# Kernel optimization log

Hardware: AMD Instinct MI355X
Metric: run time of the kernel (lower is better)

Reference implementation:

```python
import jax, jax.numpy as jnp
import numpy as np

NC = 4        # num_components
HEADS = 24
DH = 64
D = HEADS * DH  # 1536
EPS = 1e-8


def setup_inputs() -> dict:
    key = jax.random.key(0)
    ks = jax.random.split(key, 7)
    btc, S, E = 4, 4096, 154
    w = lambda k: jax.random.normal(k, (D, D), jnp.float32) * 0.02
    return {
        "hidden_states": jax.random.normal(ks[0], (btc, S, D), jnp.float32),
        "encoder_hidden_states": jax.random.normal(ks[1], (btc, E, D), jnp.float32),
        "temperature": jnp.ones((1,), jnp.float32),
        "Wq": w(ks[2]),
        "Wk": w(ks[3]),
        "Wv": w(ks[4]),
        "Wo": w(ks[5]),
        "bo": jnp.zeros((D,), jnp.float32),
        "pad_length": 154,
    }


def reference(hidden_states, encoder_hidden_states, temperature, Wq, Wk, Wv, Wo, bo, pad_length):
    btc, S, d = hidden_states.shape          # batch*components, latent seq, hidden
    E = encoder_hidden_states.shape[1]       # encoder seq (== pad_length)
    b = btc // NC
    scale = DH ** -0.5
    residual = hidden_states

    def heads(x, L):  # [btc, L, D] -> [btc, H, L, dh]
        return x.reshape(btc, L, HEADS, DH).transpose(0, 2, 1, 3)

    q = heads(hidden_states @ Wq.T, S)
    k = heads(encoder_hidden_states @ Wk.T, E)
    v = heads(encoder_hidden_states @ Wv.T, E)

    # pad tokens are zeros projected through the same k/v weights (no bias -> zeros)
    pad_h = jnp.zeros((btc, pad_length, d), hidden_states.dtype)
    k_pad = heads(pad_h @ Wk.T, pad_length)
    v_pad = heads(pad_h @ Wv.T, pad_length)

    scores = jnp.einsum('bhsd,bhed->bhse', q, k) / (temperature[0] + EPS)
    scores_pad = jnp.einsum('bhsd,bhpd->bhsp', q, k_pad) * scale

    # cross-component softmax over dim 0
    scores = scores.reshape(NC, b, HEADS, S, E)
    scores_pad = scores_pad.reshape(NC, b, HEADS, S, pad_length)
    w = jax.nn.softmax(scores, axis=0)
    w_pad = jax.nn.softmax(scores_pad, axis=0) * (NC / pad_length) * (1.0 - w)

    weights = jnp.concatenate(
        [w.reshape(btc, HEADS, S, E), w_pad.reshape(btc, HEADS, S, pad_length)],
        axis=-1)                              # [btc, H, S, E+pad]
    v_cat = jnp.concatenate([v, v_pad], axis=2)  # [btc, H, E+pad, dh]

    out = jnp.einsum('bhse,bhed->bhsd', weights, v_cat)
    out = out.transpose(0, 2, 1, 3).reshape(btc, S, d)
    out = out @ Wo.T + bo
    return out + residual
```

## Files before the change

kernel.cpp:

```cpp
#include <hip/hip_runtime.h>

typedef __attribute__((ext_vector_type(8))) short short8;
typedef __attribute__((ext_vector_type(4))) float f32x4;
typedef __attribute__((ext_vector_type(4))) unsigned short us4;
typedef __attribute__((ext_vector_type(4))) float float4v;

#define GLB_PTR(p) ((const __attribute__((address_space(1))) void*)(p))
#define LDS_PTR(p) ((__attribute__((address_space(3))) void*)(p))

__device__ __forceinline__ unsigned short f2bf(float f) {
  unsigned int u = __float_as_uint(f);
  u += 0x7FFF + ((u >> 16) & 1);
  return (unsigned short)(u >> 16);
}

__global__ void cvt_all(const float* __restrict__ i0, const float* __restrict__ i1,
                        const float* __restrict__ i2, const float* __restrict__ i3,
                        const float* __restrict__ i4, const float* __restrict__ i5,
                        unsigned short* __restrict__ o0, unsigned short* __restrict__ o1,
                        unsigned short* __restrict__ o2, unsigned short* __restrict__ o3,
                        unsigned short* __restrict__ o4, unsigned short* __restrict__ o5) {
  const float* in; unsigned short* out; int n4;
  switch (blockIdx.y) {
    case 0:  in = i0; out = o0; n4 = 16384 * 1536 / 4; break;
    case 1:  in = i1; out = o1; n4 = 616 * 1536 / 4;   break;
    case 2:  in = i2; out = o2; n4 = 1536 * 1536 / 4;  break;
    case 3:  in = i3; out = o3; n4 = 1536 * 1536 / 4;  break;
    case 4:  in = i4; out = o4; n4 = 1536 * 1536 / 4;  break;
    default: in = i5; out = o5; n4 = 1536 * 1536 / 4;  break;
  }
  int i = blockIdx.x * blockDim.x + threadIdx.x;
  int stride = gridDim.x * blockDim.x;
  for (; i < n4; i += stride) {
    float4v v = *(const float4v*)(in + (size_t)i * 4);
    us4 o;
    o[0] = f2bf(v[0]); o[1] = f2bf(v[1]); o[2] = f2bf(v[2]); o[3] = f2bf(v[3]);
    *(us4*)(out + (size_t)i * 4) = o;
  }
}

template<int MODE>
__device__ __forceinline__ void gemm_big_body(
    const unsigned short* __restrict__ A,
    const unsigned short* __restrict__ B,
    unsigned short* __restrict__ Cb,
    float* __restrict__ Cf,
    const float* __restrict__ bias,
    const float* __restrict__ resid,
    unsigned short* smem, int bid, int tid) {
  constexpr int K = 1536, N = 1536, BK = 32, NKT = K / BK;
  unsigned short* As = smem;
  unsigned short* Bs = smem + 3 * 8192;

  const int xcd = bid & 7, idx = bid >> 3;
  const int m0 = (xcd * 8 + idx / 12) * 256;
  const int n0 = (idx % 12) * 128;

  const int w = tid >> 6, l = tid & 63, lr = l & 15, lg = l >> 4;
  const int wr = w >> 1, wc = w & 1;
  const int ga = lg ^ (lr & 3);

  const int srow = w * 16 + (l >> 2);
  const int sg = (l & 3) ^ ((l >> 2) & 3);
  const unsigned short* aSrc = A + (size_t)(m0 + srow) * K + sg * 8;
  const unsigned short* bSrc = B + (size_t)(n0 + srow) * K + sg * 8;

  f32x4 acc[4][4] = {};

  auto stage = [&](int buf, int kt) {
    const int k0 = kt * BK;
    unsigned short* AsW = As + buf * 8192 + w * 512;
    unsigned short* BsW = Bs + buf * 4096 + w * 512;
    __builtin_amdgcn_global_load_lds(GLB_PTR(aSrc + k0),                    LDS_PTR(AsW),        16, 0, 0);
    __builtin_amdgcn_global_load_lds(GLB_PTR(aSrc + (size_t)128 * K + k0),  LDS_PTR(AsW + 4096), 16, 0, 0);
    __builtin_amdgcn_global_load_lds(GLB_PTR(bSrc + k0),                    LDS_PTR(BsW),        16, 0, 0);
  };

  auto loadfrags = [&](int buf, short8* af, short8* bfv) {
    const unsigned short* Asb = As + buf * 8192;
    const unsigned short* Bsb = Bs + buf * 4096;
#pragma unroll
    for (int i = 0; i < 4; ++i)
      af[i] = *(const short8*)(Asb + (wr * 64 + i * 16 + lr) * 32 + ga * 8);
#pragma unroll
    for (int j = 0; j < 4; ++j)
      bfv[j] = *(const short8*)(Bsb + (wc * 64 + j * 16 + lr) * 32 + ga * 8);
  };

  auto mfma_all = [&](short8* af, short8* bfv) {
#pragma unroll
    for (int i = 0; i < 4; ++i)
#pragma unroll
      for (int j = 0; j < 4; ++j)
        acc[i][j] = __builtin_amdgcn_mfma_f32_16x16x32_bf16(af[i], bfv[j], acc[i][j], 0, 0, 0);
  };

  stage(0, 0); stage(1, 1); stage(2, 2);

  int cur = 0;
  for (int kt = 0; kt < NKT - 3; ++kt) {
    asm volatile("s_waitcnt vmcnt(6)" ::: "memory");
    __builtin_amdgcn_s_barrier();
    __builtin_amdgcn_sched_barrier(0);
    short8 af[4], bfv[4];
    loadfrags(cur, af, bfv);
    asm volatile("s_waitcnt lgkmcnt(0)" ::: "memory");
    __builtin_amdgcn_sched_barrier(0);
    __builtin_amdgcn_s_barrier();
    __builtin_amdgcn_sched_barrier(0);
    stage(cur, kt + 3);
    __builtin_amdgcn_s_setprio(1);
    mfma_all(af, bfv);
    __builtin_amdgcn_s_setprio(0);
    cur = cur + 1; if (cur == 3) cur = 0;
  }
#pragma unroll
  for (int j = 0; j < 3; ++j) {
    if (j == 0)      asm volatile("s_waitcnt vmcnt(6)" ::: "memory");
    else if (j == 1) asm volatile("s_waitcnt vmcnt(3)" ::: "memory");
    else             asm volatile("s_waitcnt vmcnt(0)" ::: "memory");
    __builtin_amdgcn_s_barrier();
    __builtin_amdgcn_sched_barrier(0);
    short8 af[4], bfv[4];
    loadfrags(cur, af, bfv);
    mfma_all(af, bfv);
    cur = cur + 1; if (cur == 3) cur = 0;
  }

#pragma unroll
  for (int i = 0; i < 4; ++i) {
    const int rb = m0 + wr * 64 + i * 16 + lg * 4;
#pragma unroll
    for (int j = 0; j < 4; ++j) {
      const int col = n0 + wc * 64 + j * 16 + lr;
#pragma unroll
      for (int r = 0; r < 4; ++r) {
        size_t o = (size_t)(rb + r) * N + col;
        if (MODE == 0) Cb[o] = f2bf(acc[i][j][r]);
        else           Cf[o] = acc[i][j][r] + bias[col] + resid[o];
      }
    }
  }
}

__device__ __forceinline__ void gemm_kv_body(
    const unsigned short* __restrict__ A,
    const unsigned short* __restrict__ Bk,
    const unsigned short* __restrict__ Bv,
    unsigned short* __restrict__ Ck,
    unsigned short* __restrict__ Vt,
    unsigned short* smem, int by, int tid) {
  constexpr int K = 1536, N = 1536, Mc = 615;
  unsigned short* As = smem;
  unsigned short* Bs = smem + 4096;
  const int bx = by % 5, yy = by / 5;
  const unsigned short* B = yy < 12 ? Bk : Bv;
  const int m0 = bx * 128, n0 = (yy % 12) * 128;
  const bool act = tid < 256;
  const int t = tid;
  const int w = t >> 6, l = t & 63, lr = l & 15, lg = l >> 4;
  const int wr = w >> 1, wc = w & 1;
  const int srow = t >> 2, scol = (t & 3) * 8;

  f32x4 acc[4][4] = {};
  unsigned short* AsW = As + w * 512;
  unsigned short* BsW = Bs + w * 512;
  long ar0 = m0 + srow;       if (ar0 > Mc) ar0 = Mc;
  long ar1 = m0 + srow + 64;  if (ar1 > Mc) ar1 = Mc;

  for (int k0 = 0; k0 < K; k0 += 32) {
    if (act) {
      __builtin_amdgcn_global_load_lds(GLB_PTR(A + ar0 * (long)K + k0 + scol), LDS_PTR(AsW),        16, 0, 0);
      __builtin_amdgcn_global_load_lds(GLB_PTR(A + ar1 * (long)K + k0 + scol), LDS_PTR(AsW + 2048), 16, 0, 0);
      __builtin_amdgcn_global_load_lds(GLB_PTR(B + (long)(n0 + srow) * K + k0 + scol),      LDS_PTR(BsW),        16, 0, 0);
      __builtin_amdgcn_global_load_lds(GLB_PTR(B + (long)(n0 + srow + 64) * K + k0 + scol), LDS_PTR(BsW + 2048), 16, 0, 0);
    }
    __syncthreads();
    if (act) {
      short8 af[4], bfv[4];
#pragma unroll
      for (int i = 0; i < 4; ++i) {
        af[i]  = *(const short8*)(As + (wr * 64 + i * 16 + lr) * 32 + lg * 8);
        bfv[i] = *(const short8*)(Bs + (wc * 64 + i * 16 + lr) * 32 + lg * 8);
      }
#pragma unroll
      for (int i = 0; i < 4; ++i)
#pragma unroll
        for (int j = 0; j < 4; ++j)
          acc[i][j] = __builtin_amdgcn_mfma_f32_16x16x32_bf16(af[i], bfv[j], acc[i][j], 0, 0, 0);
    }
    __syncthreads();
  }

  if (!act) return;
  if (yy < 12) {
#pragma unroll
    for (int i = 0; i < 4; ++i) {
      int rb = m0 + wr * 64 + i * 16 + lg * 4;
#pragma unroll
      for (int j = 0; j < 4; ++j) {
        int col = n0 + wc * 64 + j * 16 + lr;
#pragma unroll
        for (int r = 0; r < 4; ++r)
          Ck[(long)(rb + r) * N + col] = f2bf(acc[i][j][r]);
      }
    }
  } else {
#pragma unroll
    for (int i = 0; i < 4; ++i) {
      int rb = m0 + wr * 64 + i * 16 + lg * 4;
#pragma unroll
      for (int j = 0; j < 4; ++j) {
        int col = n0 + wc * 64 + j * 16 + lr;
        int hh = col >> 6, dd = col & 63;
#pragma unroll
        for (int r = 0; r < 4; ++r) {
          int m = rb + r;
          if (m < 616) {
            int c = (unsigned)m / 154u;
            int e = m - c * 154;
            Vt[((long)((c * 24 + hh) * 64 + dd)) * 160 + e] = f2bf(acc[i][j][r]);
          }
        }
      }
    }
  }
}

__global__ __launch_bounds__(512, 4) void gemm_q_kv(
    const unsigned short* __restrict__ HSb, const unsigned short* __restrict__ Wqb,
    unsigned short* __restrict__ Qb,
    const unsigned short* __restrict__ EHSb, const unsigned short* __restrict__ Wkb,
    const unsigned short* __restrict__ Wvb,
    unsigned short* __restrict__ Ck, unsigned short* __restrict__ Vt) {
  __shared__ unsigned short smem[36864];
  if (blockIdx.x < 768)
    gemm_big_body<0>(HSb, Wqb, Qb, nullptr, nullptr, nullptr, smem, blockIdx.x, threadIdx.x);
  else
    gemm_kv_body(EHSb, Wkb, Wvb, Ck, Vt, smem, blockIdx.x - 768, threadIdx.x);
}

__global__ __launch_bounds__(512, 4) void gemm_o(
    const unsigned short* __restrict__ Ob, const unsigned short* __restrict__ Wob,
    float* __restrict__ Cf, const float* __restrict__ bias, const float* __restrict__ resid) {
  __shared__ unsigned short smem[36864];
  gemm_big_body<1>(Ob, Wob, nullptr, Cf, bias, resid, smem, blockIdx.x, threadIdx.x);
}

__global__ __launch_bounds__(256) void attn_kernel(
    const unsigned short* __restrict__ Qb,
    const unsigned short* __restrict__ Kb,
    const unsigned short* __restrict__ Vt,
    const float* __restrict__ temp,
    unsigned short* __restrict__ Ob) {
  __shared__ unsigned short P[4][4][16][160];
  const int h = blockIdx.y, sb = blockIdx.x;
  const int t = threadIdx.x, w = t >> 6, l = t & 63, lr = l & 15, lg = l >> 4;
  const int s0 = sb * 64 + w * 16;
  const float sc = 1.0f / (temp[0] + 1e-8f);

  short8 qf[4][2];
#pragma unroll
  for (int c = 0; c < 4; ++c)
#pragma unroll
    for (int kt = 0; kt < 2; ++kt)
      qf[c][kt] = *(const short8*)(Qb + (long)(c * 4096 + s0 + lr) * 1536 + h * 64 + kt * 32 + lg * 8);

  short8 kA[4][2], kB[4][2];
  auto loadK = [&](int et, short8 (&k)[4][2]) {
#pragma unroll
    for (int c = 0; c < 4; ++c)
#pragma unroll
      for (int kt = 0; kt < 2; ++kt)
        k[c][kt] = *(const short8*)(Kb + (long)(c * 154 + et * 16 + lr) * 1536 + h * 64 + kt * 32 + lg * 8);
  };

  auto qk_step = [&](int et, short8 (&kc)[4][2], short8 (&kn)[4][2], bool pre) {
    if (pre) loadK(et + 1, kn);
    f32x4 sa[4] = {};
#pragma unroll
    for (int c = 0; c < 4; ++c)
#pragma unroll
      for (int kt = 0; kt < 2; ++kt)
        sa[c] = __builtin_amdgcn_mfma_f32_16x16x32_bf16(kc[c][kt], qf[c][kt], sa[c], 0, 0, 0);
    float wv[4][4];
#pragma unroll
    for (int r = 0; r < 4; ++r) {
      float e0 = __expf(sa[0][r] * sc), e1 = __expf(sa[1][r] * sc);
      float e2 = __expf(sa[2][r] * sc), e3 = __expf(sa[3][r] * sc);
      float inv = 1.0f / (e0 + e1 + e2 + e3);
      wv[0][r] = e0 * inv; wv[1][r] = e1 * inv; wv[2][r] = e2 * inv; wv[3][r] = e3 * inv;
    }
#pragma unroll
    for (int c = 0; c < 4; ++c) {
      us4 pk;
#pragma unroll
      for (int r = 0; r < 4; ++r)
        pk[r] = (et * 16 + lg * 4 + r < 154) ? f2bf(wv[c][r]) : (unsigned short)0;
      *(us4*)&P[w][c][lr][et * 16 + lg * 4] = pk;
    }
  };

  loadK(0, kA);
#pragma unroll
  for (int et = 0; et < 10; et += 2) {
    qk_step(et,     kA, kB, true);
    qk_step(et + 1, kB, kA, et + 1 < 9);
  }
  __syncthreads();

  short8 vA[4], vB[4];
  auto loadV = [&](int c, int ks, short8 (&v)[4]) {
#pragma unroll
    for (int nt = 0; nt < 4; ++nt)
      v[nt] = *(const short8*)(Vt + (long)((c * 24 + h) * 64 + nt * 16 + lr) * 160 + ks * 32 + lg * 8);
  };

  f32x4 o[4][4] = {};
  loadV(0, 0, vA);
#pragma unroll
  for (int p = 0; p < 10; ++p) {
    const int i0 = 2 * p, i1 = 2 * p + 1;
    const int c0 = i0 / 5, k0 = i0 % 5;
    const int c1 = i1 / 5, k1 = i1 % 5;
    loadV(c1, k1, vB);
    short8 pf0 = *(const short8*)&P[w][c0][lr][k0 * 32 + lg * 8];
#pragma unroll
    for (int nt = 0; nt < 4; ++nt)
      o[c0][nt] = __builtin_amdgcn_mfma_f32_16x16x32_bf16(pf0, vA[nt], o[c0][nt], 0, 0, 0);
    if (p < 9) loadV((i1 + 1) / 5, (i1 + 1) % 5, vA);
    short8 pf1 = *(const short8*)&P[w][c1][lr][k1 * 32 + lg * 8];
#pragma unroll
    for (int nt = 0; nt < 4; ++nt)
      o[c1][nt] = __builtin_amdgcn_mfma_f32_16x16x32_bf16(pf1, vB[nt], o[c1][nt], 0, 0, 0);
  }

#pragma unroll
  for (int c = 0; c < 4; ++c)
#pragma unroll
    for (int nt = 0; nt < 4; ++nt)
#pragma unroll
      for (int r = 0; r < 4; ++r)
        Ob[(long)(c * 4096 + s0 + lg * 4 + r) * 1536 + h * 64 + nt * 16 + lr] = f2bf(o[c][nt][r]);
}

extern "C" void kernel_launch(void* const* d_in, const int* in_sizes, int n_in,
                              void* d_out, int out_size, void* d_ws, size_t ws_size,
                              hipStream_t stream) {
  (void)in_sizes; (void)n_in; (void)out_size; (void)ws_size;
  const float* HS  = (const float*)d_in[0];
  const float* EHS = (const float*)d_in[1];
  const float* TMP = (const float*)d_in[2];
  const float* Wq  = (const float*)d_in[3];
  const float* Wk  = (const float*)d_in[4];
  const float* Wv  = (const float*)d_in[5];
  const float* Wo  = (const float*)d_in[6];
  const float* bo  = (const float*)d_in[7];

  char* ws = (char*)d_ws;
  size_t off = 0;
  unsigned short* HSb  = (unsigned short*)(ws + off); off += (size_t)16384 * 1536 * 2;
  unsigned short* Ob   = HSb;
  unsigned short* EHSb = (unsigned short*)(ws + off); off += (size_t)616 * 1536 * 2;
  unsigned short* Wqb  = (unsigned short*)(ws + off); off += (size_t)1536 * 1536 * 2;
  unsigned short* Wkb  = (unsigned short*)(ws + off); off += (size_t)1536 * 1536 * 2;
  unsigned short* Wvb  = (unsigned short*)(ws + off); off += (size_t)1536 * 1536 * 2;
  unsigned short* Wob  = (unsigned short*)(ws + off); off += (size_t)1536 * 1536 * 2;
  unsigned short* Kb   = (unsigned short*)(ws + off); off += (size_t)640 * 1536 * 2;
  unsigned short* Vt   = (unsigned short*)(ws + off); off += (size_t)4 * 24 * 64 * 160 * 2;
  unsigned short* Qb   = (unsigned short*)d_out;

  cvt_all<<<dim3(1024, 6), 256, 0, stream>>>(HS, EHS, Wq, Wk, Wv, Wo,
                                             HSb, EHSb, Wqb, Wkb, Wvb, Wob);

  gemm_q_kv<<<888, 512, 0, stream>>>(HSb, Wqb, Qb, EHSb, Wkb, Wvb, Kb, Vt);

  attn_kernel<<<dim3(64, 24), 256, 0, stream>>>(Qb, Kb, Vt, TMP, Ob);

  gemm_o<<<768, 512, 0, stream>>>(Ob, Wob, (float*)d_out, bo, HS);
}
```

Measured before the change: 356.6 us.

## Use 4-wave GEMM blocks with 128x64 per-wave tiles and double buffering

The big GEMM (Q projection and output projection) moves from 8 waves each computing 64x64 to 4 waves each computing 128x64 of the same 256x128 block tile. Each wave now holds 32 accumulators, so loaded fragments are reused across more MFMAs. The LDS pipeline drops from triple to double buffering to cut shared memory, and the K/V GEMM path drops its idle-thread guard to fit 256-thread blocks. The trade-off is higher register pressure and fewer resident waves, with less latency hiding from the shallower prefetch.

```diff
diff --git a/kernel.cpp b/kernel.cpp
--- a/kernel.cpp
+++ b/kernel.cpp
@@ -50,7 +50,7 @@
     unsigned short* smem, int bid, int tid) {
   constexpr int K = 1536, N = 1536, BK = 32, NKT = K / BK;
   unsigned short* As = smem;
-  unsigned short* Bs = smem + 3 * 8192;
+  unsigned short* Bs = smem + 2 * 8192;
 
   const int xcd = bid & 7, idx = bid >> 3;
   const int m0 = (xcd * 8 + idx / 12) * 256;
@@ -60,28 +60,31 @@
   const int wr = w >> 1, wc = w & 1;
   const int ga = lg ^ (lr & 3);
 
-  const int srow = w * 16 + (l >> 2);
-  const int sg = (l & 3) ^ ((l >> 2) & 3);
+  const int srow = tid >> 2;
+  const int sg = (tid & 3) ^ (srow & 3);
   const unsigned short* aSrc = A + (size_t)(m0 + srow) * K + sg * 8;
   const unsigned short* bSrc = B + (size_t)(n0 + srow) * K + sg * 8;
 
-  f32x4 acc[4][4] = {};
+  f32x4 acc[8][4] = {};
 
   auto stage = [&](int buf, int kt) {
     const int k0 = kt * BK;
     unsigned short* AsW = As + buf * 8192 + w * 512;
     unsigned short* BsW = Bs + buf * 4096 + w * 512;
-    __builtin_amdgcn_global_load_lds(GLB_PTR(aSrc + k0),                    LDS_PTR(AsW),        16, 0, 0);
-    __builtin_amdgcn_global_load_lds(GLB_PTR(aSrc + (size_t)128 * K + k0),  LDS_PTR(AsW + 4096), 16, 0, 0);
-    __builtin_amdgcn_global_load_lds(GLB_PTR(bSrc + k0),                    LDS_PTR(BsW),        16, 0, 0);
+#pragma unroll
+    for (int i = 0; i < 4; ++i)
+      __builtin_amdgcn_global_load_lds(GLB_PTR(aSrc + (size_t)(i * 64) * K + k0), LDS_PTR(AsW + i * 2048), 16, 0, 0);
+#pragma unroll
+    for (int i = 0; i < 2; ++i)
+      __builtin_amdgcn_global_load_lds(GLB_PTR(bSrc + (size_t)(i * 64) * K + k0), LDS_PTR(BsW + i * 2048), 16, 0, 0);
   };
 
   auto loadfrags = [&](int buf, short8* af, short8* bfv) {
     const unsigned short* Asb = As + buf * 8192;
     const unsigned short* Bsb = Bs + buf * 4096;
 #pragma unroll
-    for (int i = 0; i < 4; ++i)
-      af[i] = *(const short8*)(Asb + (wr * 64 + i * 16 + lr) * 32 + ga * 8);
+    for (int i = 0; i < 8; ++i)
+      af[i] = *(const short8*)(Asb + (wr * 128 + i * 16 + lr) * 32 + ga * 8);
 #pragma unroll
     for (int j = 0; j < 4; ++j)
       bfv[j] = *(const short8*)(Bsb + (wc * 64 + j * 16 + lr) * 32 + ga * 8);
@@ -89,47 +92,34 @@
 
   auto mfma_all = [&](short8* af, short8* bfv) {
 #pragma unroll
-    for (int i = 0; i < 4; ++i)
+    for (int i = 0; i < 8; ++i)
 #pragma unroll
       for (int j = 0; j < 4; ++j)
         acc[i][j] = __builtin_amdgcn_mfma_f32_16x16x32_bf16(af[i], bfv[j], acc[i][j], 0, 0, 0);
   };
 
-  stage(0, 0); stage(1, 1); stage(2, 2);
-
-  int cur = 0;
-  for (int kt = 0; kt < NKT - 3; ++kt) {
-    asm volatile("s_waitcnt vmcnt(6)" ::: "memory");
+  stage(0, 0); stage(1, 1);
+
+  for (int kt = 0; kt < NKT; ++kt) {
+    if (kt < NKT - 1) asm volatile("s_waitcnt vmcnt(6)" ::: "memory");
+    else              asm volatile("s_waitcnt vmcnt(0)" ::: "memory");
     __builtin_amdgcn_s_barrier();
     __builtin_amdgcn_sched_barrier(0);
-    short8 af[4], bfv[4];
-    loadfrags(cur, af, bfv);
+    short8 af[8], bfv[4];
+    loadfrags(kt & 1, af, bfv);
     asm volatile("s_waitcnt lgkmcnt(0)" ::: "memory");
     __builtin_amdgcn_sched_barrier(0);
     __builtin_amdgcn_s_barrier();
     __builtin_amdgcn_sched_barrier(0);
-    stage(cur, kt + 3);
+    if (kt + 2 < NKT) stage(kt & 1, kt + 2);
     __builtin_amdgcn_s_setprio(1);
     mfma_all(af, bfv);
     __builtin_amdgcn_s_setprio(0);
-    cur = cur + 1; if (cur == 3) cur = 0;
-  }
-#pragma unroll
-  for (int j = 0; j < 3; ++j) {
-    if (j == 0)      asm volatile("s_waitcnt vmcnt(6)" ::: "memory");
-    else if (j == 1) asm volatile("s_waitcnt vmcnt(3)" ::: "memory");
-    else             asm volatile("s_waitcnt vmcnt(0)" ::: "memory");
-    __builtin_amdgcn_s_barrier();
-    __builtin_amdgcn_sched_barrier(0);
-    short8 af[4], bfv[4];
-    loadfrags(cur, af, bfv);
-    mfma_all(af, bfv);
-    cur = cur + 1; if (cur == 3) cur = 0;
-  }
-
-#pragma unroll
-  for (int i = 0; i < 4; ++i) {
-    const int rb = m0 + wr * 64 + i * 16 + lg * 4;
+  }
+
+#pragma unroll
+  for (int i = 0; i < 8; ++i) {
+    const int rb = m0 + wr * 128 + i * 16 + lg * 4;
 #pragma unroll
     for (int j = 0; j < 4; ++j) {
       const int col = n0 + wc * 64 + j * 16 + lr;
@@ -156,7 +146,6 @@
   const int bx = by % 5, yy = by / 5;
   const unsigned short* B = yy < 12 ? Bk : Bv;
   const int m0 = bx * 128, n0 = (yy % 12) * 128;
-  const bool act = tid < 256;
   const int t = tid;
   const int w = t >> 6, l = t & 63, lr = l & 15, lg = l >> 4;
   const int wr = w >> 1, wc = w & 1;
@@ -169,30 +158,26 @@
   long ar1 = m0 + srow + 64;  if (ar1 > Mc) ar1 = Mc;
 
   for (int k0 = 0; k0 < K; k0 += 32) {
-    if (act) {
-      __builtin_amdgcn_global_load_lds(GLB_PTR(A + ar0 * (long)K + k0 + scol), LDS_PTR(AsW),        16, 0, 0);
-      __builtin_amdgcn_global_load_lds(GLB_PTR(A + ar1 * (long)K + k0 + scol), LDS_PTR(AsW + 2048), 16, 0, 0);
-      __builtin_amdgcn_global_load_lds(GLB_PTR(B + (long)(n0 + srow) * K + k0 + scol),      LDS_PTR(BsW),        16, 0, 0);
-      __builtin_amdgcn_global_load_lds(GLB_PTR(B + (long)(n0 + srow + 64) * K + k0 + scol), LDS_PTR(BsW + 2048), 16, 0, 0);
-    }
+    __builtin_amdgcn_global_load_lds(GLB_PTR(A + ar0 * (long)K + k0 + scol), LDS_PTR(AsW),        16, 0, 0);
+    __builtin_amdgcn_global_load_lds(GLB_PTR(A + ar1 * (long)K + k0 + scol), LDS_PTR(AsW + 2048), 16, 0, 0);
+    __builtin_amdgcn_global_load_lds(GLB_PTR(B + (long)(n0 + srow) * K + k0 + scol),      LDS_PTR(BsW),        16, 0, 0);
+    __builtin_amdgcn_global_load_lds(GLB_PTR(B + (long)(n0 + srow + 64) * K + k0 + scol), LDS_PTR(BsW + 2048), 16, 0, 0);
     __syncthreads();
-    if (act) {
-      short8 af[4], bfv[4];
-#pragma unroll
-      for (int i = 0; i < 4; ++i) {
-        af[i]  = *(const short8*)(As + (wr * 64 + i * 16 + lr) * 32 + lg * 8);
-        bfv[i] = *(const short8*)(Bs + (wc * 64 + i * 16 + lr) * 32 + lg * 8);
-      }
-#pragma unroll
-      for (int i = 0; i < 4; ++i)
-#pragma unroll
-        for (int j = 0; j < 4; ++j)
-          acc[i][j] = __builtin_amdgcn_mfma_f32_16x16x32_bf16(af[i], bfv[j], acc[i][j], 0, 0, 0);
-    }
+
+    short8 af[4], bfv[4];
+#pragma unroll
+    for (int i = 0; i < 4; ++i) {
+      af[i]  = *(const short8*)(As + (wr * 64 + i * 16 + lr) * 32 + lg * 8);
+      bfv[i] = *(const short8*)(Bs + (wc * 64 + i * 16 + lr) * 32 + lg * 8);
+    }
+#pragma unroll
+    for (int i = 0; i < 4; ++i)
+#pragma unroll
+      for (int j = 0; j < 4; ++j)
+        acc[i][j] = __builtin_amdgcn_mfma_f32_16x16x32_bf16(af[i], bfv[j], acc[i][j], 0, 0, 0);
     __syncthreads();
   }
 
-  if (!act) return;
   if (yy < 12) {
 #pragma unroll
     for (int i = 0; i < 4; ++i) {
@@ -227,23 +212,23 @@
   }
 }
 
-__global__ __launch_bounds__(512, 4) void gemm_q_kv(
+__global__ __launch_bounds__(256, 3) void gemm_q_kv(
     const unsigned short* __restrict__ HSb, const unsigned short* __restrict__ Wqb,
     unsigned short* __restrict__ Qb,
     const unsigned short* __restrict__ EHSb, const unsigned short* __restrict__ Wkb,
     const unsigned short* __restrict__ Wvb,
     unsigned short* __restrict__ Ck, unsigned short* __restrict__ Vt) {
-  __shared__ unsigned short smem[36864];
+  __shared__ unsigned short smem[24576];
   if (blockIdx.x < 768)
     gemm_big_body<0>(HSb, Wqb, Qb, nullptr, nullptr, nullptr, smem, blockIdx.x, threadIdx.x);
   else
     gemm_kv_body(EHSb, Wkb, Wvb, Ck, Vt, smem, blockIdx.x - 768, threadIdx.x);
 }
 
-__global__ __launch_bounds__(512, 4) void gemm_o(
+__global__ __launch_bounds__(256, 3) void gemm_o(
     const unsigned short* __restrict__ Ob, const unsigned short* __restrict__ Wob,
     float* __restrict__ Cf, const float* __restrict__ bias, const float* __restrict__ resid) {
-  __shared__ unsigned short smem[36864];
+  __shared__ unsigned short smem[24576];
   gemm_big_body<1>(Ob, Wob, nullptr, Cf, bias, resid, smem, blockIdx.x, threadIdx.x);
 }
 
@@ -373,9 +358,9 @@
   cvt_all<<<dim3(1024, 6), 256, 0, stream>>>(HS, EHS, Wq, Wk, Wv, Wo,
                                              HSb, EHSb, Wqb, Wkb, Wvb, Wob);
 
-  gemm_q_kv<<<888, 512, 0, stream>>>(HSb, Wqb, Qb, EHSb, Wkb, Wvb, Kb, Vt);
+  gemm_q_kv<<<888, 256, 0, stream>>>(HSb, Wqb, Qb, EHSb, Wkb, Wvb, Kb, Vt);
 
   attn_kernel<<<dim3(64, 24), 256, 0, stream>>>(Qb, Kb, Vt, TMP, Ob);
 
-  gemm_o<<<768, 512, 0, stream>>>(Ob, Wob, (float*)d_out, bo, HS);
-}
+  gemm_o<<<768, 256, 0, stream>>>(Ob, Wob, (float*)d_out, bo, HS);
+}
```

Result: slower. 628.1 us (+76.1%).
